# Kernel optimization log

Hardware: AMD Instinct MI355X
Metric: run time of the kernel (lower is better)

The kernel has to match this reference:

```python
import jax, jax.numpy as jnp
import numpy as np

N_HEAD, D_HEAD = 16, 64
D_MODEL = N_HEAD * D_HEAD
QLEN, MLEN, BSZ = 1024, 1024, 4
KLEN = QLEN + MLEN
LN_EPS = 1e-5


def setup_inputs() -> dict:
    key = jax.random.key(0)
    ks = jax.random.split(key, 8)
    w = jax.random.normal(ks[0], (QLEN, BSZ, D_MODEL), jnp.float32)
    r = jax.random.normal(ks[1], (KLEN, D_MODEL), jnp.float32)
    mems = jax.random.normal(ks[2], (MLEN, BSZ, D_MODEL), jnp.float32)
    # causal mask over (qlen, klen): query i may attend keys j <= i + MLEN
    i = jnp.arange(QLEN)[:, None]
    j = jnp.arange(KLEN)[None, :]
    attn_mask = j > (i + MLEN)  # True = masked
    s = 1.0 / np.sqrt(D_MODEL)
    qkv_w = jax.random.normal(ks[3], (3 * D_MODEL, D_MODEL), jnp.float32) * s
    r_net_w = jax.random.normal(ks[4], (D_MODEL, D_MODEL), jnp.float32) * s
    o_w = jax.random.normal(ks[5], (D_MODEL, D_MODEL), jnp.float32) * s
    r_r_bias = jax.random.normal(ks[6], (N_HEAD, D_HEAD), jnp.float32) * 0.02
    r_w_bias = jax.random.normal(ks[7], (N_HEAD, D_HEAD), jnp.float32) * 0.02
    ln_gamma = jnp.ones((D_MODEL,), jnp.float32)
    ln_beta = jnp.zeros((D_MODEL,), jnp.float32)
    return {"w": w, "r": r, "mems": mems, "attn_mask": attn_mask,
            "qkv_w": qkv_w, "r_net_w": r_net_w, "o_w": o_w,
            "r_r_bias": r_r_bias, "r_w_bias": r_w_bias,
            "ln_gamma": ln_gamma, "ln_beta": ln_beta}


def _layer_norm(x, g, b):
    mu = jnp.mean(x, axis=-1, keepdims=True)
    var = jnp.var(x, axis=-1, keepdims=True)
    return (x - mu) * jax.lax.rsqrt(var + LN_EPS) * g + b


def _rel_shift(x):
    # x: [qlen, rlen, bsz, n_head]
    q, rl, b, n = x.shape
    x_pad = jnp.pad(x, ((0, 0), (1, 0), (0, 0), (0, 0)))  # zero row at front of axis 1
    x_pad = x_pad.reshape(rl + 1, q, b, n)
    return x_pad[1:].reshape(q, rl, b, n)


def reference(w, r, mems, attn_mask, qkv_w, r_net_w, o_w, r_r_bias, r_w_bias, ln_gamma, ln_beta):
    qlen, bsz = w.shape[0], w.shape[1]
    cat = jnp.concatenate([mems, w], axis=0)  # [klen, b, d]
    klen = cat.shape[0]
    w_heads = cat @ qkv_w.T  # [klen, b, 3*d]
    r_head_k = (r @ r_net_w.T).reshape(r.shape[0], N_HEAD, D_HEAD)  # [rlen, n, dh]
    w_q, w_k, w_v = jnp.split(w_heads, 3, axis=-1)
    w_q = w_q[-qlen:].reshape(qlen, bsz, N_HEAD, D_HEAD)
    w_k = w_k.reshape(klen, bsz, N_HEAD, D_HEAD)
    w_v = w_v.reshape(klen, bsz, N_HEAD, D_HEAD)

    scale = 1.0 / np.sqrt(D_HEAD)
    AC = jnp.einsum('ibnd,jbnd->ijbn', w_q + r_w_bias, w_k)
    BD = _rel_shift(jnp.einsum('ibnd,jnd->ijbn', w_q + r_r_bias, r_head_k))
    attn_score = (AC + BD) * scale
    attn_score = jnp.where(attn_mask[None, :, :, None].transpose(1, 2, 0, 3), -1e30, attn_score) if False else \
        jnp.where(attn_mask[:, :, None, None], jnp.float32(-1e30), attn_score)
    attn_prob = jax.nn.softmax(attn_score, axis=1)
    attn_vec = jnp.einsum('ijbn,jbnd->ibnd', attn_prob, w_v)
    attn_vec = attn_vec.reshape(qlen, bsz, N_HEAD * D_HEAD)
    attn_out = attn_vec @ o_w.T
    return _layer_norm(w + attn_out, ln_gamma, ln_beta)
```

## Files before the change

kernel.cpp:

```cpp
#include <hip/hip_runtime.h>
#include <hip/hip_bf16.h>

typedef __attribute__((ext_vector_type(8))) short short8;
typedef __attribute__((ext_vector_type(4))) float f32x4;
typedef __hip_bfloat16 bf16;

#define NHEAD 16
#define DHEAD 64
#define DMODEL 1024
#define QLEN 1024
#define MLEN 1024
#define BSZ 4
#define KLEN 2048
#define LOG2E 1.44269504088896f

__device__ __forceinline__ float fast_exp2(float x) {
#if __has_builtin(__builtin_amdgcn_exp2f)
  return __builtin_amdgcn_exp2f(x);
#else
  return exp2f(x);
#endif
}

__device__ __forceinline__ short8 ld8(const bf16* p) { return *(const short8*)p; }
__device__ __forceinline__ void st8(bf16* p, short8 v) { *(short8*)p = v; }
__device__ __forceinline__ f32x4 mfma16(short8 a, short8 b, f32x4 c) {
  return __builtin_amdgcn_mfma_f32_16x16x32_bf16(a, b, c, 0, 0, 0);
}
__device__ __forceinline__ float bfu2f(unsigned short u) {
  unsigned int x = ((unsigned int)u) << 16;
  return __uint_as_float(x);
}
__device__ __forceinline__ unsigned short f2bfu(float f) {
  bf16 t = __float2bfloat16(f);
  return *(unsigned short*)&t;
}
__device__ __forceinline__ unsigned short f2bfu_fast(float f) {
  return (unsigned short)((__float_as_uint(f) + 0x8000u) >> 16);
}
__device__ __forceinline__ bf16 bf16_raw(unsigned short u) {
  bf16 t; *(unsigned short*)&t = u; return t;
}
__device__ __forceinline__ void async16(const bf16* g, bf16* l) {
  __builtin_amdgcn_global_load_lds(
      (const __attribute__((address_space(1))) unsigned int*)g,
      (__attribute__((address_space(3))) unsigned int*)l, 16, 0, 0);
}

#define DPPF(x, ctrl, rm) \
  __int_as_float(__builtin_amdgcn_update_dpp( \
      __float_as_int(x), __float_as_int(x), (ctrl), (rm), 0xF, false))

__global__ void detect_dtype(const unsigned short* wq, int* flag) {
  const int tid = threadIdx.x;
  int cnt = 0;
  #pragma unroll
  for (int j = 0; j < 8; ++j) {
    unsigned short u = wq[2 * (tid * 8 + j)];
    int e = (u >> 7) & 0xFF;
    if (e >= 100 && e <= 134) cnt++;
  }
  #pragma unroll
  for (int o = 32; o > 0; o >>= 1) cnt += __shfl_xor(cnt, o, 64);
  __shared__ int red[4];
  if ((tid & 63) == 0) red[tid >> 6] = cnt;
  __syncthreads();
  if (tid == 0) {
    int total = red[0] + red[1] + red[2] + red[3];
    *flag = (total > 1024) ? 0 : 1;
  }
}

__global__ __launch_bounds__(256) void convert_inputs(
    const void* s0, const void* s1, const void* s2,
    const void* s3, const void* s4, const void* s5,
    bf16* d0, bf16* d1, bf16* d2, bf16* d3, bf16* d4, bf16* d5,
    const int* flag)
{
  const int b = blockIdx.x;
  const void* src; bf16* dst; int lb;
  if (b < 2048)      { src = s0; dst = d0; lb = b; }
  else if (b < 4096) { src = s1; dst = d1; lb = b - 2048; }
  else if (b < 5120) { src = s2; dst = d2; lb = b - 4096; }
  else if (b < 6656) { src = s3; dst = d3; lb = b - 5120; }
  else if (b < 7168) { src = s4; dst = d4; lb = b - 6656; }
  else               { src = s5; dst = d5; lb = b - 7168; }
  const size_t idx = ((size_t)lb * 256 + threadIdx.x) * 8;
  if (*flag) {
    const f32x4* f = (const f32x4*)src;
    f32x4 a = f[idx >> 2];
    f32x4 c = f[(idx >> 2) + 1];
    short8 v;
    v[0] = (short)f2bfu(a[0]); v[1] = (short)f2bfu(a[1]);
    v[2] = (short)f2bfu(a[2]); v[3] = (short)f2bfu(a[3]);
    v[4] = (short)f2bfu(c[0]); v[5] = (short)f2bfu(c[1]);
    v[6] = (short)f2bfu(c[2]); v[7] = (short)f2bfu(c[3]);
    st8(dst + idx, v);
  } else {
    st8(dst + idx, ld8((const bf16*)src + idx));
  }
}

__device__ __forceinline__ void gemm_core64(
    const bf16* const ap[4], const bf16* const bp[4],
    bf16* As, bf16* Bs, int wv, int wm, int wn, int lr, int lg,
    f32x4 acc[4][4])
{
  const int sx = lr & 7;
  for (int k0 = 0; k0 < DMODEL; k0 += 64) {
    #pragma unroll
    for (int p = 0; p < 4; ++p) {
      async16(ap[p] + k0, As + (wv * 32 + p * 8) * 64);
      async16(bp[p] + k0, Bs + (wv * 32 + p * 8) * 64);
    }
    __syncthreads();
    #pragma unroll
    for (int ks = 0; ks < 2; ++ks) {
      const int col = (((ks * 4 + lg) ^ sx) << 3);
      short8 af[4], bfr[4];
      #pragma unroll
      for (int mt = 0; mt < 4; ++mt) af[mt] = ld8(As + (wm * 64 + mt * 16 + lr) * 64 + col);
      #pragma unroll
      for (int nt = 0; nt < 4; ++nt) bfr[nt] = ld8(Bs + (wn * 64 + nt * 16 + lr) * 64 + col);
      #pragma unroll
      for (int mt = 0; mt < 4; ++mt)
        #pragma unroll
        for (int nt = 0; nt < 4; ++nt)
          acc[mt][nt] = mfma16(af[mt], bfr[nt], acc[mt][nt]);
    }
    __syncthreads();
  }
}

__global__ __launch_bounds__(256) void qkv_gemm(
    const bf16* __restrict__ w, const bf16* __restrict__ mems,
    const bf16* __restrict__ qkv_w,
    const bf16* __restrict__ r, const bf16* __restrict__ rnet_w,
    const void* __restrict__ r_w_bias, const void* __restrict__ r_r_bias,
    const int* __restrict__ flag,
    bf16* __restrict__ qac, bf16* __restrict__ qbd,
    bf16* __restrict__ kbuf, bf16* __restrict__ vbuf,
    bf16* __restrict__ rkbuf)
{
  const int id = blockIdx.x;
  int sec, bx, by;
  if (id < 256)       { sec = 0; bx = id >> 5;                    by = 32 + (id & 31); }
  else if (id < 768)  { sec = 1; int t = id - 256;  bx = 8  + (t >> 6); by = t & 63; }
  else if (id < 1280) { sec = 2; int t = id - 768;  bx = 16 + (t >> 6); by = t & 63; }
  else                { sec = 3; int t = id - 1280; bx = 24 + (t >> 4); by = t & 15; }
  __shared__ bf16 sh[16384];
  bf16* As = sh;
  bf16* Bs = sh + 8192;
  const int tid = threadIdx.x;
  const int lane = tid & 63, wv = tid >> 6;
  const int wm = wv >> 1, wn = wv & 1;
  const int lr = lane & 15, lg = lane >> 4;
  const int lr8 = lane >> 3;
  const int ucol = ((lane & 7) ^ lr8) * 8;
  const bf16 *ap[4], *bp[4];
  #pragma unroll
  for (int p = 0; p < 4; ++p) {
    int arow = wv * 32 + p * 8 + lr8;
    if (sec == 3) {
      ap[p] = r + (size_t)(by * 128 + arow) * DMODEL + ucol;
      bp[p] = rnet_w + (size_t)((bx - 24) * 128 + arow) * DMODEL + ucol;
    } else {
      int m = by * 128 + arow;
      int j = m >> 2, b = m & 3;
      ap[p] = ((j < MLEN) ? (mems + ((size_t)(j * BSZ + b)) * DMODEL)
                          : (w + ((size_t)((j - MLEN) * BSZ + b)) * DMODEL)) + ucol;
      bp[p] = qkv_w + (size_t)(bx * 128 + arow) * DMODEL + ucol;
    }
  }
  f32x4 zero = {0.f, 0.f, 0.f, 0.f};
  f32x4 acc[4][4];
  #pragma unroll
  for (int a = 0; a < 4; ++a)
    #pragma unroll
    for (int c2 = 0; c2 < 4; ++c2) acc[a][c2] = zero;
  gemm_core64(ap, bp, As, Bs, wv, wm, wn, lr, lg, acc);

  if (sec == 2) {
    #pragma unroll
    for (int nt = 0; nt < 4; ++nt) {
      int n = wn * 64 + nt * 16 + lr;
      #pragma unroll
      for (int mt = 0; mt < 4; ++mt) {
        int jl = wm * 16 + mt * 4 + lg;
        #pragma unroll
        for (int rr = 0; rr < 4; ++rr) {
          int x = rr * 32 + jl;
          sh[n * 128 + (((x >> 4) ^ (n & 7)) << 4) + (x & 15)] =
              __float2bfloat16(acc[mt][nt][rr]);
        }
      }
    }
    __syncthreads();
    const int grp = lane >> 3, sl = lane & 7;
    const int hbase = (bx - 16) * 2;
    #pragma unroll
    for (int i = 0; i < 16; ++i) {
      int idx = i * 32 + wv * 8 + grp;
      int n = idx >> 2, bb = idx & 3;
      int x0 = bb * 32 + sl * 4;
      ushort4 v4 = *(const ushort4*)(sh + n * 128 + (((x0 >> 4) ^ (n & 7)) << 4) + (x0 & 15));
      int hh = hbase + (n >> 6), dd = n & 63;
      *(ushort4*)(vbuf + ((size_t)(bb * NHEAD + hh) * DHEAD + dd) * KLEN + by * 32 + sl * 4) = v4;
    }
    return;
  }
  if (sec == 3) {
    #pragma unroll
    for (int nt = 0; nt < 4; ++nt) {
      int col = (bx - 24) * 128 + wn * 64 + nt * 16 + lr;
      int h = col >> 6, d = col & 63;
      #pragma unroll
      for (int mt = 0; mt < 4; ++mt) {
        #pragma unroll
        for (int rr = 0; rr < 4; ++rr) {
          int m = by * 128 + wm * 64 + mt * 16 + lg * 4 + rr;
          rkbuf[((size_t)h * KLEN + m) * DHEAD + d] = __float2bfloat16(acc[mt][nt][rr]);
        }
      }
    }
    return;
  }
  const int isf = (sec == 0) ? *flag : 0;
  const float QSC = 0.125f * LOG2E;
  #pragma unroll
  for (int nt = 0; nt < 4; ++nt) {
    int col = bx * 128 + wn * 64 + nt * 16 + lr;
    int nn = col & 1023;
    int h = nn >> 6, d = nn & 63;
    float rwb = 0.f, rrb = 0.f;
    if (sec == 0) {
      if (isf) { rwb = ((const float*)r_w_bias)[nn]; rrb = ((const float*)r_r_bias)[nn]; }
      else { rwb = __bfloat162float(((const bf16*)r_w_bias)[nn]);
             rrb = __bfloat162float(((const bf16*)r_r_bias)[nn]); }
    }
    #pragma unroll
    for (int mt = 0; mt < 4; ++mt) {
      #pragma unroll
      for (int rr = 0; rr < 4; ++rr) {
        int m = by * 128 + wm * 64 + mt * 16 + lg * 4 + rr;
        int j = m >> 2, b = m & 3;
        float v = acc[mt][nt][rr];
        if (sec == 0) {
          int i = j - MLEN;
          size_t base = (((size_t)(b * NHEAD + h)) * QLEN + i) * DHEAD + d;
          qac[base] = __float2bfloat16((v + rwb) * QSC);
          qbd[base] = __float2bfloat16((v + rrb) * QSC);
        } else {
          kbuf[(((size_t)(b * NHEAD + h)) * KLEN + j) * DHEAD + d] = __float2bfloat16(v);
        }
      }
    }
  }
}

#define RRBODY(RR, CTRL) { \
    const int di = g * 4 + RR; \
    float sh[5]; \
    _Pragma("unroll") for (int ct = 0; ct < 5; ++ct) { \
      float y = Gr[ct][RR]; \
      sh[ct] = __int_as_float(__builtin_amdgcn_update_dpp( \
          __float_as_int(y), __float_as_int(y), (CTRL), 0xF, 0xF, false)); \
    } \
    float sv[4]; \
    _Pragma("unroll") for (int jt = 0; jt < 4; ++jt) { \
      float bd = (c > di) ? sh[jt + 1] : sh[jt]; \
      sv[jt] = S[jt][RR] + bd; \
    } \
    if (lastt) { \
      const int ig = i0 + wv * 16 + di; \
      _Pragma("unroll") for (int jt = 0; jt < 4; ++jt) \
        if (j0 + jt * 16 + c > ig + MLEN) sv[jt] = -1e30f; \
    } \
    _Pragma("unroll") for (int jt = 0; jt < 4; ++jt) { \
      float pv = fast_exp2(sv[jt]); \
      ls[RR] += pv; \
      pw[di * 64 + ((((jt * 2) + (c >> 3)) ^ (di & 7)) << 3) + (c & 7)] = \
          bf16_raw(f2bfu_fast(pv)); \
    } \
  }

__global__ __launch_bounds__(256, 4) void attn_kernel(
    const bf16* __restrict__ qac, const bf16* __restrict__ qbd,
    const bf16* __restrict__ kbuf, const bf16* __restrict__ vbuf,
    const bf16* __restrict__ rkbuf, bf16* __restrict__ av)
{
  const int id = blockIdx.x;
  const int qt = 15 - (id >> 6);
  const int bh = id & 63;
  const int b = bh >> 4, h = bh & 15;
  const int i0 = qt * 64;
  __shared__ bf16 Ks[64 * 64];
  __shared__ bf16 Vt[64 * 64];
  __shared__ bf16 Rs[192 * 64];
  __shared__ bf16 Ps[4 * 16 * 64];
  const int tid = threadIdx.x;
  const int wv = tid >> 6, lane = tid & 63;
  const int c = lane & 15, g = lane >> 4;
  const size_t bhb = (size_t)(b * NHEAD + h);
  const int lr8 = lane >> 3;
  const int ucol = ((lane & 7) ^ lr8) * 8;
  const int sw0 = ((0 + g) ^ (c & 7)) * 8;
  const int sw1 = ((4 + g) ^ (c & 7)) * 8;

  short8 qaf[2], qbf[2];
  {
    const size_t qrow = (bhb * QLEN + i0 + wv * 16 + c) * DHEAD;
    #pragma unroll
    for (int ks = 0; ks < 2; ++ks) {
      qaf[ks] = ld8(qac + qrow + ks * 32 + g * 8);
      qbf[ks] = ld8(qbd + qrow + ks * 32 + g * 8);
    }
  }
  f32x4 zero = {0.f, 0.f, 0.f, 0.f};
  f32x4 O[4];
  #pragma unroll
  for (int dt = 0; dt < 4; ++dt) O[dt] = zero;
  float ls[4] = {0.f, 0.f, 0.f, 0.f};

  bf16* pw = Ps + wv * (16 * 64);
  const bf16* kc = Ks + c * 64;
  const bf16* vc = Vt + c * 64;

  const int relb = c + 48 - wv * 16;
  int loSw[2][5];
  #pragma unroll
  for (int ks = 0; ks < 2; ++ks)
    #pragma unroll
    for (int ct = 0; ct < 5; ++ct) {
      int rel = relb + ct * 16;
      loSw[ks][ct] = (rel & 63) * 64 + (ks ? sw1 : sw0);
    }

  const int ntiles = qt + 17;
  const int mlo0 = 960 - i0;
  const int mb0 = (mlo0 >> 6) % 3;
  const bf16* rkh = rkbuf + (size_t)h * KLEN * DHEAD;

  #pragma unroll
  for (int p = 0; p < 2; ++p) {
    int r0 = wv * 16 + p * 8;
    async16(kbuf + (bhb * KLEN + r0 + lr8) * DHEAD + ucol, Ks + r0 * 64);
    async16(vbuf + (bhb * DHEAD + r0 + lr8) * KLEN + ucol, Vt + r0 * 64);
  }
  #pragma unroll
  for (int p = 0; p < 4; ++p) {
    int rr = wv * 32 + p * 8;
    int bank = ((rr >> 6) ? ((mb0 + 1) % 3) : mb0) * 4096;
    async16(rkh + (size_t)(mlo0 + rr + lr8) * DHEAD + ucol,
            Rs + bank + (rr & 63) * 64);
  }
  {
    const int bank2 = ((mb0 + 2) % 3) * 4096;
    #pragma unroll
    for (int p = 0; p < 2; ++p) {
      int rw = wv * 16 + p * 8;
      async16(rkh + (size_t)(mlo0 + 128 + rw + lr8) * DHEAD + ucol,
              Rs + bank2 + rw * 64);
    }
  }

  int b0e = mb0 * 4096;
  int b1e = ((mb0 + 1) % 3) * 4096;

  for (int t = 0; t < ntiles; ++t) {
    const int j0 = t * 64;
    const int m_lo = mlo0 + j0;
    if (t + 1 < ntiles) {
      asm volatile("s_waitcnt vmcnt(2)" ::: "memory");
    } else {
      asm volatile("s_waitcnt vmcnt(0)" ::: "memory");
    }
    __builtin_amdgcn_s_barrier();
    __builtin_amdgcn_sched_barrier(0);

    f32x4 S[4], G[5];
    #pragma unroll
    for (int jt = 0; jt < 4; ++jt) S[jt] = zero;
    #pragma unroll
    for (int ct = 0; ct < 5; ++ct) G[ct] = zero;
    const bf16* rb0 = Rs + b0e;
    const bf16* rb1 = Rs + b1e;
    #pragma unroll
    for (int ks = 0; ks < 2; ++ks) {
      const int sw = ks ? sw1 : sw0;
      #pragma unroll
      for (int jt = 0; jt < 4; ++jt)
        S[jt] = mfma16(qaf[ks], ld8(kc + jt * 1024 + sw), S[jt]);
      #pragma unroll
      for (int ct = 0; ct < 5; ++ct)
        G[ct] = mfma16(qbf[ks], ld8((ct > wv ? rb1 : rb0) + loSw[ks][ct]), G[ct]);
    }
    float Gr[5][4];
    #pragma unroll
    for (int ct = 0; ct < 5; ++ct)
      #pragma unroll
      for (int rr = 0; rr < 4; ++rr) {
        float y = G[ct][rr];
        y = DPPF(y, 0x124, 0xA);
        y = DPPF(y, 0x128, 0xC);
        Gr[ct][rr] = y;
      }
    const bool lastt = (t == ntiles - 1);
    RRBODY(0, 0x121)
    RRBODY(1, 0x122)
    RRBODY(2, 0x123)
    RRBODY(3, 0x124)
    #pragma unroll
    for (int ks = 0; ks < 2; ++ks) {
      short8 pf = ld8(pw + c * 64 + (((ks * 4 + g) ^ (c & 7)) << 3));
      const int sw = ks ? sw1 : sw0;
      #pragma unroll
      for (int dt = 0; dt < 4; ++dt)
        O[dt] = mfma16(pf, ld8(vc + dt * 1024 + sw), O[dt]);
    }
    asm volatile("s_waitcnt lgkmcnt(0)" ::: "memory");
    __builtin_amdgcn_s_barrier();
    __builtin_amdgcn_sched_barrier(0);
    if (t + 1 < ntiles) {
      const int j1 = j0 + 64;
      #pragma unroll
      for (int p = 0; p < 2; ++p) {
        int r0 = wv * 16 + p * 8;
        async16(kbuf + (bhb * KLEN + j1 + r0 + lr8) * DHEAD + ucol, Ks + r0 * 64);
        async16(vbuf + (bhb * DHEAD + r0 + lr8) * KLEN + j1 + ucol, Vt + r0 * 64);
      }
    }
    if (t + 2 < ntiles) {
      #pragma unroll
      for (int p = 0; p < 2; ++p) {
        int rw = wv * 16 + p * 8;
        async16(rkh + (size_t)(m_lo + 192 + rw + lr8) * DHEAD + ucol,
                Rs + b0e + rw * 64);
      }
    }
    int nb = b1e + 4096; if (nb == 12288) nb = 0;
    b0e = b1e; b1e = nb;
  }
  #pragma unroll
  for (int rr = 0; rr < 4; ++rr) {
    float s = ls[rr];
    s += DPPF(s, 0xB1, 0xF);
    s += DPPF(s, 0x4E, 0xF);
    s += DPPF(s, 0x141, 0xF);
    s += DPPF(s, 0x140, 0xF);
    ls[rr] = s;
  }
  #pragma unroll
  for (int rr = 0; rr < 4; ++rr) {
    float inv = 1.0f / ls[rr];
    #pragma unroll
    for (int dt = 0; dt < 4; ++dt) {
      int ig = i0 + wv * 16 + g * 4 + rr;
      int d = dt * 16 + c;
      av[((size_t)ig * BSZ + b) * DMODEL + h * DHEAD + d] =
          __float2bfloat16(O[dt][rr] * inv);
    }
  }
}

__global__ __launch_bounds__(256) void out_gemm(
    const bf16* __restrict__ av, const bf16* __restrict__ o_w,
    bf16* __restrict__ ao)
{
  const int id = blockIdx.x;
  const int bx = id >> 5, by = id & 31;
  __shared__ bf16 As[128 * 64];
  __shared__ bf16 Bs[128 * 64];
  const int tid = threadIdx.x;
  const int lane = tid & 63, wv = tid >> 6;
  const int wm = wv >> 1, wn = wv & 1;
  const int lr = lane & 15, lg = lane >> 4;
  const int lr8 = lane >> 3;
  const int ucol = ((lane & 7) ^ lr8) * 8;
  const bf16 *ap[4], *bp[4];
  #pragma unroll
  for (int p = 0; p < 4; ++p) {
    int arow = wv * 32 + p * 8 + lr8;
    ap[p] = av + (size_t)(by * 128 + arow) * DMODEL + ucol;
    bp[p] = o_w + (size_t)(bx * 128 + arow) * DMODEL + ucol;
  }
  f32x4 zero = {0.f, 0.f, 0.f, 0.f};
  f32x4 acc[4][4];
  #pragma unroll
  for (int a = 0; a < 4; ++a)
    #pragma unroll
    for (int c2 = 0; c2 < 4; ++c2) acc[a][c2] = zero;
  gemm_core64(ap, bp, As, Bs, wv, wm, wn, lr, lg, acc);
  #pragma unroll
  for (int nt = 0; nt < 4; ++nt) {
    int col = bx * 128 + wn * 64 + nt * 16 + lr;
    #pragma unroll
    for (int mt = 0; mt < 4; ++mt) {
      #pragma unroll
      for (int rr = 0; rr < 4; ++rr) {
        int m = by * 128 + wm * 64 + mt * 16 + lg * 4 + rr;
        ao[(size_t)m * DMODEL + col] = __float2bfloat16(acc[mt][nt][rr]);
      }
    }
  }
}

__global__ __launch_bounds__(256) void ln_kernel(
    const void* __restrict__ wz, const bf16* __restrict__ ao,
    const void* __restrict__ gz, const void* __restrict__ bz,
    void* __restrict__ outz, const int* __restrict__ flag)
{
  const int m = blockIdx.x;
  const int tid = threadIdx.x;
  const int isf = *flag;
  ushort4 au = ((const ushort4*)ao)[m * 256 + tid];
  float a4[4];
  a4[0] = bfu2f(au.x); a4[1] = bfu2f(au.y); a4[2] = bfu2f(au.z); a4[3] = bfu2f(au.w);
  float x[4], gg[4], bb[4];
  if (isf) {
    f32x4 w4 = ((const f32x4*)wz)[m * 256 + tid];
    f32x4 g4 = ((const f32x4*)gz)[tid];
    f32x4 b4 = ((const f32x4*)bz)[tid];
    #pragma unroll
    for (int k = 0; k < 4; ++k) { x[k] = w4[k] + a4[k]; gg[k] = g4[k]; bb[k] = b4[k]; }
  } else {
    ushort4 w4 = ((const ushort4*)wz)[m * 256 + tid];
    ushort4 g4 = ((const ushort4*)gz)[tid];
    ushort4 b4 = ((const ushort4*)bz)[tid];
    x[0] = bfu2f(w4.x) + a4[0]; x[1] = bfu2f(w4.y) + a4[1];
    x[2] = bfu2f(w4.z) + a4[2]; x[3] = bfu2f(w4.w) + a4[3];
    gg[0] = bfu2f(g4.x); gg[1] = bfu2f(g4.y); gg[2] = bfu2f(g4.z); gg[3] = bfu2f(g4.w);
    bb[0] = bfu2f(b4.x); bb[1] = bfu2f(b4.y); bb[2] = bfu2f(b4.z); bb[3] = bfu2f(b4.w);
  }
  float s = x[0] + x[1] + x[2] + x[3];
  float s2 = x[0]*x[0] + x[1]*x[1] + x[2]*x[2] + x[3]*x[3];
  #pragma unroll
  for (int o = 32; o > 0; o >>= 1) {
    s += __shfl_xor(s, o, 64);
    s2 += __shfl_xor(s2, o, 64);
  }
  __shared__ float red[8];
  const int wv = tid >> 6, lane = tid & 63;
  if (lane == 0) { red[wv] = s; red[4 + wv] = s2; }
  __syncthreads();
  s = red[0] + red[1] + red[2] + red[3];
  s2 = red[4] + red[5] + red[6] + red[7];
  const float mu = s * (1.0f / DMODEL);
  const float var = s2 * (1.0f / DMODEL) - mu * mu;
  const float rstd = rsqrtf(var + 1e-5f);
  float y[4];
  #pragma unroll
  for (int k = 0; k < 4; ++k) y[k] = (x[k] - mu) * rstd * gg[k] + bb[k];
  if (isf) {
    f32x4 o4; o4[0] = y[0]; o4[1] = y[1]; o4[2] = y[2]; o4[3] = y[3];
    ((f32x4*)outz)[m * 256 + tid] = o4;
  } else {
    ushort4 o4;
    o4.x = f2bfu(y[0]); o4.y = f2bfu(y[1]); o4.z = f2bfu(y[2]); o4.w = f2bfu(y[3]);
    ((ushort4*)outz)[m * 256 + tid] = o4;
  }
}

extern "C" void kernel_launch(void* const* d_in, const int* in_sizes, int n_in,
                              void* d_out, int out_size, void* d_ws, size_t ws_size,
                              hipStream_t stream) {
  (void)in_sizes; (void)n_in; (void)out_size; (void)ws_size;
  const void* w      = d_in[0];
  const void* r      = d_in[1];
  const void* mems   = d_in[2];
  const void* qkv_w  = d_in[4];
  const void* rnet_w = d_in[5];
  const void* o_w    = d_in[6];
  const void* rrb    = d_in[7];
  const void* rwb    = d_in[8];
  const void* ln_g   = d_in[9];
  const void* ln_b   = d_in[10];

  char* ws = (char*)d_ws;
  const size_t MB = 1ull << 20;
  bf16* cw    = (bf16*)(ws + 0 * MB);
  bf16* cmems = (bf16*)(ws + 8 * MB);
  bf16* cr    = (bf16*)(ws + 16 * MB);
  bf16* cqkvw = (bf16*)(ws + 20 * MB);
  bf16* crnet = (bf16*)(ws + 26 * MB);
  bf16* cow   = (bf16*)(ws + 28 * MB);
  int*  flag  = (int*)(ws + 30 * MB);
  bf16* qac   = (bf16*)(ws + 31 * MB);
  bf16* qbd   = (bf16*)(ws + 39 * MB);
  bf16* kbuf  = (bf16*)(ws + 47 * MB);
  bf16* vbuf  = (bf16*)(ws + 63 * MB);
  bf16* rkbuf = (bf16*)(ws + 79 * MB);
  bf16* av    = (bf16*)(ws + 83 * MB);
  bf16* ao    = (bf16*)(ws + 0 * MB);

  detect_dtype<<<1, 256, 0, stream>>>((const unsigned short*)w, flag);
  convert_inputs<<<7680, 256, 0, stream>>>(w, mems, r, qkv_w, rnet_w, o_w,
                                           cw, cmems, cr, cqkvw, crnet, cow, flag);
  qkv_gemm<<<1408, 256, 0, stream>>>(cw, cmems, cqkvw, cr, crnet,
                                     rwb, rrb, flag,
                                     qac, qbd, kbuf, vbuf, rkbuf);
  attn_kernel<<<1024, 256, 0, stream>>>(qac, qbd, kbuf, vbuf, rkbuf, av);
  out_gemm<<<256, 256, 0, stream>>>(av, cow, ao);
  ln_kernel<<<dim3(4096), 256, 0, stream>>>(w, ao, ln_g, ln_b, d_out, flag);
}
```

Baseline: 296.1 us.

## Split K/R and V prefetch phases and shrink R ring to double buffer

Replaces the three-bank rolling R-key buffer with a two-bank ping-pong, which cuts LDS use by 8 KB per block. K and R loads for the next tile are now issued right after the score MFMAs, behind an added barrier. V loads are issued after the PV MFMAs. The aim is to overlap each prefetch with a different compute phase and possibly raise occupancy, at the cost of an extra barrier per tile and shorter prefetch lead time for R.

```diff
diff --git a/kernel.cpp b/kernel.cpp
--- a/kernel.cpp
+++ b/kernel.cpp
@@ -296,7 +296,7 @@
   const int i0 = qt * 64;
   __shared__ bf16 Ks[64 * 64];
   __shared__ bf16 Vt[64 * 64];
-  __shared__ bf16 Rs[192 * 64];
+  __shared__ bf16 Rs[128 * 64];
   __shared__ bf16 Ps[4 * 16 * 64];
   const int tid = threadIdx.x;
   const int wv = tid >> 6, lane = tid & 63;
@@ -338,43 +338,30 @@
 
   const int ntiles = qt + 17;
   const int mlo0 = 960 - i0;
-  const int mb0 = (mlo0 >> 6) % 3;
   const bf16* rkh = rkbuf + (size_t)h * KLEN * DHEAD;
 
   #pragma unroll
   for (int p = 0; p < 2; ++p) {
     int r0 = wv * 16 + p * 8;
     async16(kbuf + (bhb * KLEN + r0 + lr8) * DHEAD + ucol, Ks + r0 * 64);
-    async16(vbuf + (bhb * DHEAD + r0 + lr8) * KLEN + ucol, Vt + r0 * 64);
   }
   #pragma unroll
   for (int p = 0; p < 4; ++p) {
     int rr = wv * 32 + p * 8;
-    int bank = ((rr >> 6) ? ((mb0 + 1) % 3) : mb0) * 4096;
-    async16(rkh + (size_t)(mlo0 + rr + lr8) * DHEAD + ucol,
-            Rs + bank + (rr & 63) * 64);
-  }
-  {
-    const int bank2 = ((mb0 + 2) % 3) * 4096;
-    #pragma unroll
-    for (int p = 0; p < 2; ++p) {
-      int rw = wv * 16 + p * 8;
-      async16(rkh + (size_t)(mlo0 + 128 + rw + lr8) * DHEAD + ucol,
-              Rs + bank2 + rw * 64);
-    }
-  }
-
-  int b0e = mb0 * 4096;
-  int b1e = ((mb0 + 1) % 3) * 4096;
+    async16(rkh + (size_t)(mlo0 + rr + lr8) * DHEAD + ucol, Rs + rr * 64);
+  }
+  #pragma unroll
+  for (int p = 0; p < 2; ++p) {
+    int r0 = wv * 16 + p * 8;
+    async16(vbuf + (bhb * DHEAD + r0 + lr8) * KLEN + ucol, Vt + r0 * 64);
+  }
+
+  int b0e = 0, b1e = 4096;
 
   for (int t = 0; t < ntiles; ++t) {
     const int j0 = t * 64;
     const int m_lo = mlo0 + j0;
-    if (t + 1 < ntiles) {
-      asm volatile("s_waitcnt vmcnt(2)" ::: "memory");
-    } else {
-      asm volatile("s_waitcnt vmcnt(0)" ::: "memory");
-    }
+    asm volatile("s_waitcnt vmcnt(2)" ::: "memory");
     __builtin_amdgcn_s_barrier();
     __builtin_amdgcn_sched_barrier(0);
 
@@ -394,6 +381,20 @@
       #pragma unroll
       for (int ct = 0; ct < 5; ++ct)
         G[ct] = mfma16(qbf[ks], ld8((ct > wv ? rb1 : rb0) + loSw[ks][ct]), G[ct]);
+    }
+    asm volatile("s_waitcnt vmcnt(0) lgkmcnt(0)" ::: "memory");
+    __builtin_amdgcn_s_barrier();
+    __builtin_amdgcn_sched_barrier(0);
+    if (t + 1 < ntiles) {
+      const int j1 = j0 + 64;
+      #pragma unroll
+      for (int p = 0; p < 2; ++p) {
+        int r0 = wv * 16 + p * 8;
+        async16(kbuf + (bhb * KLEN + j1 + r0 + lr8) * DHEAD + ucol, Ks + r0 * 64);
+        async16(rkh + (size_t)(m_lo + 128 + r0 + lr8) * DHEAD + ucol,
+                Rs + b0e + r0 * 64);
+      }
+      __builtin_amdgcn_sched_barrier(0);
     }
     float Gr[5][4];
     #pragma unroll
@@ -418,28 +419,18 @@
       for (int dt = 0; dt < 4; ++dt)
         O[dt] = mfma16(pf, ld8(vc + dt * 1024 + sw), O[dt]);
     }
-    asm volatile("s_waitcnt lgkmcnt(0)" ::: "memory");
-    __builtin_amdgcn_s_barrier();
-    __builtin_amdgcn_sched_barrier(0);
     if (t + 1 < ntiles) {
+      asm volatile("s_waitcnt lgkmcnt(0)" ::: "memory");
+      __builtin_amdgcn_s_barrier();
+      __builtin_amdgcn_sched_barrier(0);
       const int j1 = j0 + 64;
       #pragma unroll
       for (int p = 0; p < 2; ++p) {
         int r0 = wv * 16 + p * 8;
-        async16(kbuf + (bhb * KLEN + j1 + r0 + lr8) * DHEAD + ucol, Ks + r0 * 64);
         async16(vbuf + (bhb * DHEAD + r0 + lr8) * KLEN + j1 + ucol, Vt + r0 * 64);
       }
     }
-    if (t + 2 < ntiles) {
-      #pragma unroll
-      for (int p = 0; p < 2; ++p) {
-        int rw = wv * 16 + p * 8;
-        async16(rkh + (size_t)(m_lo + 192 + rw + lr8) * DHEAD + ucol,
-                Rs + b0e + rw * 64);
-      }
-    }
-    int nb = b1e + 4096; if (nb == 12288) nb = 0;
-    b0e = b1e; b1e = nb;
+    int tb = b0e; b0e = b1e; b1e = tb;
   }
   #pragma unroll
   for (int rr = 0; rr < 4; ++rr) {
```

After: 289.9 us. 1.02x faster.
